# Performance work log

Hardware: AMD Instinct MI355X
Metric: run time of the kernel (lower is better)

## Reference

```python
import jax, jax.numpy as jnp
import numpy as np

B, N, NUM_BUCKETS = 16, 2048, 128
TS_MAX = 10_000_000


def _bucketize(dt):
    # log2 bucketization of timestamp deltas: floor(log2(max(|dt|, 1)))
    return jnp.floor(
        jnp.log(jnp.maximum(jnp.abs(dt).astype(jnp.float32), 1.0)) / jnp.log(2.0)
    ).astype(jnp.int32)


def setup_inputs() -> dict:
    key = jax.random.key(0)
    k1, k2, k3 = jax.random.split(key, 3)
    all_timestamps = jnp.sort(
        jax.random.randint(k1, (B, N), 0, TS_MAX, dtype=jnp.int32), axis=-1
    )
    pos_w = 0.02 * jax.random.normal(k2, (2 * N - 1,), dtype=jnp.float32)
    ts_w = 0.02 * jax.random.normal(k3, (NUM_BUCKETS + 1,), dtype=jnp.float32)
    return {"all_timestamps": all_timestamps, "pos_w": pos_w, "ts_w": ts_w}


def reference(all_timestamps, pos_w, ts_w):
    b, n = all_timestamps.shape
    num_buckets = ts_w.shape[0] - 1

    # --- relative position bias ---
    # The torch pad/repeat/reshape/slice Toeplitz trick is equivalent to
    # rel_pos_bias[i, j] = pos_w[(N-1) + j - i], since the flat index
    # (i*(3N-2) + (N-1) + j) mod (3N-1) == (N-1) + j - i  for |j-i| <= N-1.
    idx = (n - 1) + jnp.arange(n)[None, :] - jnp.arange(n)[:, None]  # (N, N)
    rel_pos_bias = pos_w[idx][None]  # (1, N, N)

    # --- bucketized timestamp bias ---
    # use_action == False path: append last timestamp.
    ext = jnp.concatenate([all_timestamps, all_timestamps[:, n - 1 : n]], axis=1)  # (B, N+1)
    dt = ext[:, 1:, None] - ext[:, None, :-1]  # (B, N, N)
    bucketed = jnp.clip(_bucketize(dt), 0, num_buckets)  # indices are non-diff (detach)
    rel_ts_bias = ts_w[bucketed]  # (B, N, N) gather

    return rel_pos_bias, rel_ts_bias
```

## Files before the change

kernel.cpp:

```cpp
#include <hip/hip_runtime.h>

constexpr int kN = 2048;
constexpr int kB = 16;
constexpr int kNB = 128;

#define LN2_BITS 0x3f317218u

__global__ __launch_bounds__(256) void pos_kernel(const float* __restrict__ pos_w,
                                                  float* __restrict__ out) {
    __shared__ float lds[2 * kN - 1];
    const int i = blockIdx.x;
    for (int t = threadIdx.x; t < 2 * kN - 1; t += 256) lds[t] = pos_w[t];
    __syncthreads();
    const int base = kN - 1 - i;
    float* __restrict__ orow = out + (size_t)i * kN;
    #pragma unroll
    for (int k = 0; k < kN / 256; ++k) {
        const int j = k * 256 + threadIdx.x;
        orow[j] = lds[base + j];
    }
}

__device__ __forceinline__ int bucket_of(int rowts, int tj) {
    int dt = rowts - tj;
    unsigned a = (unsigned)(dt < 0 ? -dt : dt);
    a = a < 1u ? 1u : a;
    int k = 31 - __clz((int)a);
    unsigned p = 1u << k;
    unsigned Wlo = ((p >> 20) * (unsigned)k) + 8u;
    unsigned Whi = ((p >> 19) * (unsigned)(k + 1)) + 8u;
    bool danger = ((a - p) < Wlo) | (((p << 1) - a) < Whi);
    if (!danger) return k;
    float L = (float)log((double)a);
    float q = L / __uint_as_float(LN2_BITS);
    int bk = (int)floorf(q);
    return bk < 0 ? 0 : (bk > kNB ? kNB : bk);
}

__global__ __launch_bounds__(256) void ts_kernel(const int* __restrict__ ts,
                                                 const float* __restrict__ ts_w,
                                                 float* __restrict__ out) {
    __shared__ float w[kNB + 1];
    if (threadIdx.x <= kNB) w[threadIdx.x] = ts_w[threadIdx.x];
    __syncthreads();

    const int bi = blockIdx.x;
    const int b  = bi >> 11;
    const int i  = bi & (kN - 1);

    const int* __restrict__ tsrow = ts + (size_t)b * kN;
    const int rowts = tsrow[min(i + 1, kN - 1)];

    const int4* __restrict__ ts4 = (const int4*)tsrow;
    float4* __restrict__ orow4 =
        (float4*)(out + (size_t)kN * kN + (size_t)bi * kN);

    #pragma unroll
    for (int kk = 0; kk < kN / (4 * 256); ++kk) {
        const int v = kk * 256 + threadIdx.x;
        const int4 t4 = ts4[v];
        float4 r;
        r.x = w[bucket_of(rowts, t4.x)];
        r.y = w[bucket_of(rowts, t4.y)];
        r.z = w[bucket_of(rowts, t4.z)];
        r.w = w[bucket_of(rowts, t4.w)];
        orow4[v] = r;
    }
}

extern "C" void kernel_launch(void* const* d_in, const int* in_sizes, int n_in,
                              void* d_out, int out_size, void* d_ws, size_t ws_size,
                              hipStream_t stream) {
    const int*   all_ts = (const int*)d_in[0];
    const float* pos_w  = (const float*)d_in[1];
    const float* ts_w   = (const float*)d_in[2];
    float* out = (float*)d_out;

    pos_kernel<<<kN, 256, 0, stream>>>(pos_w, out);
    ts_kernel<<<kB * kN, 256, 0, stream>>>(all_ts, ts_w, out);
}
```

Baseline: 58.57 us.

## Fuse position and timestamp bias kernels into one launch with nontemporal stores

Merges the two kernels into a single grid where the first B*N blocks compute timestamp-bucket bias rows and the trailing N blocks write the Toeplitz position bias. The position path now reads pos_w directly from global memory (cached) and writes 16-byte vectors instead of staging the table in LDS. All output stores use nontemporal hints to avoid polluting caches with write-only data. This removes a kernel launch and the tail gap between kernels, at the cost of unaligned scalar global loads in the position path.

After: 49.99 us (median of 2 runs). 1.17x faster.

```diff
diff --git a/kernel.cpp b/kernel.cpp
--- a/kernel.cpp
+++ b/kernel.cpp
@@ -6,20 +6,8 @@
 
 #define LN2_BITS 0x3f317218u
 
-__global__ __launch_bounds__(256) void pos_kernel(const float* __restrict__ pos_w,
-                                                  float* __restrict__ out) {
-    __shared__ float lds[2 * kN - 1];
-    const int i = blockIdx.x;
-    for (int t = threadIdx.x; t < 2 * kN - 1; t += 256) lds[t] = pos_w[t];
-    __syncthreads();
-    const int base = kN - 1 - i;
-    float* __restrict__ orow = out + (size_t)i * kN;
-    #pragma unroll
-    for (int k = 0; k < kN / 256; ++k) {
-        const int j = k * 256 + threadIdx.x;
-        orow[j] = lds[base + j];
-    }
-}
+typedef float f32x4 __attribute__((ext_vector_type(4)));
+typedef int   i32x4 __attribute__((ext_vector_type(4)));
 
 __device__ __forceinline__ int bucket_of(int rowts, int tj) {
     int dt = rowts - tj;
@@ -37,34 +25,51 @@
     return bk < 0 ? 0 : (bk > kNB ? kNB : bk);
 }
 
-__global__ __launch_bounds__(256) void ts_kernel(const int* __restrict__ ts,
-                                                 const float* __restrict__ ts_w,
-                                                 float* __restrict__ out) {
-    __shared__ float w[kNB + 1];
-    if (threadIdx.x <= kNB) w[threadIdx.x] = ts_w[threadIdx.x];
-    __syncthreads();
+__global__ __launch_bounds__(256) void bias_kernel(const int* __restrict__ ts,
+                                                   const float* __restrict__ pos_w,
+                                                   const float* __restrict__ ts_w,
+                                                   float* __restrict__ out) {
+    const int blk = blockIdx.x;
 
-    const int bi = blockIdx.x;
-    const int b  = bi >> 11;
-    const int i  = bi & (kN - 1);
+    if (blk < kB * kN) {
+        __shared__ float w[kNB + 1];
+        if (threadIdx.x <= kNB) w[threadIdx.x] = ts_w[threadIdx.x];
+        __syncthreads();
 
-    const int* __restrict__ tsrow = ts + (size_t)b * kN;
-    const int rowts = tsrow[min(i + 1, kN - 1)];
+        const int b = blk >> 11;
+        const int i = blk & (kN - 1);
+        const int* __restrict__ tsrow = ts + (size_t)b * kN;
+        const int rowts = tsrow[min(i + 1, kN - 1)];
 
-    const int4* __restrict__ ts4 = (const int4*)tsrow;
-    float4* __restrict__ orow4 =
-        (float4*)(out + (size_t)kN * kN + (size_t)bi * kN);
+        const i32x4* __restrict__ ts4 = (const i32x4*)tsrow;
+        f32x4* __restrict__ orow4 =
+            (f32x4*)(out + (size_t)kN * kN + (size_t)blk * kN);
 
-    #pragma unroll
-    for (int kk = 0; kk < kN / (4 * 256); ++kk) {
-        const int v = kk * 256 + threadIdx.x;
-        const int4 t4 = ts4[v];
-        float4 r;
-        r.x = w[bucket_of(rowts, t4.x)];
-        r.y = w[bucket_of(rowts, t4.y)];
-        r.z = w[bucket_of(rowts, t4.z)];
-        r.w = w[bucket_of(rowts, t4.w)];
-        orow4[v] = r;
+        #pragma unroll
+        for (int kk = 0; kk < kN / (4 * 256); ++kk) {
+            const int v = kk * 256 + threadIdx.x;
+            const i32x4 t4 = ts4[v];
+            f32x4 r;
+            r.x = w[bucket_of(rowts, t4.x)];
+            r.y = w[bucket_of(rowts, t4.y)];
+            r.z = w[bucket_of(rowts, t4.z)];
+            r.w = w[bucket_of(rowts, t4.w)];
+            __builtin_nontemporal_store(r, &orow4[v]);
+        }
+    } else {
+        const int i = blk - kB * kN;
+        const float* __restrict__ src = pos_w + (kN - 1 - i);
+        f32x4* __restrict__ orow4 = (f32x4*)(out + (size_t)i * kN);
+        #pragma unroll
+        for (int kk = 0; kk < kN / (4 * 256); ++kk) {
+            const int v = kk * 256 + threadIdx.x;
+            f32x4 r;
+            r.x = src[4 * v + 0];
+            r.y = src[4 * v + 1];
+            r.z = src[4 * v + 2];
+            r.w = src[4 * v + 3];
+            __builtin_nontemporal_store(r, &orow4[v]);
+        }
     }
 }
 
@@ -76,6 +81,5 @@
     const float* ts_w   = (const float*)d_in[2];
     float* out = (float*)d_out;
 
-    pos_kernel<<<kN, 256, 0, stream>>>(pos_w, out);
-    ts_kernel<<<kB * kN, 256, 0, stream>>>(all_ts, ts_w, out);
+    bias_kernel<<<kB * kN + kN, 256, 0, stream>>>(all_ts, pos_w, ts_w, out);
 }
```
